# Performance work log

Measured on AMD Instinct MI355X. Metric: run time of the kernel, lower is better.

Reference implementation:

```python
import jax, jax.numpy as jnp
import numpy as np

B, NELEC, D, NION = 2048, 32, 512, 8
NSPIN = 2
N = NELEC // NSPIN  # electrons per spin = orbital-matrix size = 16


def setup_inputs() -> dict:
    key = jax.random.key(0)
    ks = jax.random.split(key, 6)
    eq_inputs = jax.random.normal(ks[0], (B, NELEC, D), jnp.float32)
    r_ei = jax.random.normal(ks[1], (B, NELEC, NION, 3), jnp.float32)
    # learned params (stacked over the 2 spins; equal split so shapes match)
    W_lin = jax.random.normal(ks[2], (NSPIN, 2 * D, N), jnp.float32) * (0.5 / np.sqrt(D))
    b_lin = jax.random.normal(ks[3], (NSPIN, N), jnp.float32) * 0.1
    A_env = jax.random.normal(ks[4], (NSPIN, 3, 3, NION, N), jnp.float32) * 0.3
    w_ion = jax.random.normal(ks[5], (NSPIN, NION, N), jnp.float32)
    return dict(eq_inputs=eq_inputs, r_ei=r_ei, W_lin=W_lin, b_lin=b_lin,
                A_env=A_env, w_ion=w_ion)


def reference(eq_inputs, r_ei, W_lin, b_lin, A_env, w_ion):
    """Per-particle determinant antiequivariance layer.

    For each spin s and particle p, a doubly-equivariant orbital matrix
    M_p[j, k] = (y_p . W1[:,k] + y_j . W2[:,k] + b[k]) * env[j, k]
    is built (pair-concat dense split into two einsums to avoid the (B,n,n,2d)
    intermediate), with anisotropic exponential envelopes
    env[j, k] = sum_I w_ion[I,k] * exp(-||A[:,:,I,k] @ r_ei[j,I,:]||).
    Output per spin: y_p * det(M_p), stacked over spins -> (B, 2, n, d).
    """
    b, nelec, d = eq_inputs.shape
    n = nelec // NSPIN
    x = eq_inputs.reshape(b, NSPIN, n, d)            # spin_split=2 equal split
    r = r_ei.reshape(b, NSPIN, n, r_ei.shape[-2], 3)
    W1, W2 = W_lin[:, :d], W_lin[:, d:]
    # linear (doubly equivariant) part: (B, S, n_p, n_j, n_k)
    lin_p = jnp.einsum('bspf,sfk->bspk', x, W1)
    lin_j = jnp.einsum('bsjf,sfk->bsjk', x, W2) + b_lin[None, :, None, :]
    lin = lin_p[:, :, :, None, :] + lin_j[:, :, None, :, :]
    # anisotropic exponential envelopes: exp(-||A (r - R)||), combined over ions
    ar = jnp.einsum('bsjip,spqik->bsjiqk', r, A_env)        # (B,S,n,I,3,k)
    env = jnp.exp(-jnp.sqrt(jnp.sum(ar * ar, axis=-2)))     # (B,S,n,I,k)
    env = jnp.einsum('bsjik,sik->bsjk', env, w_ion)         # (B,S,n_j,n_k)
    M = lin * env[:, :, None, :, :]                         # (B,S,n_p,n_j,n_k)
    dets = jnp.linalg.det(M)                                # (B,S,n_p)
    # y_p * det(M_p), per spin (stacked over the spin axis)
    return x * dets[..., None]                              # (B,S,n,d)
```

## Files before the change

### kernel.cpp

```cpp
#include <hip/hip_runtime.h>
#include <cstdint>
#include <cstddef>

#define NSPIN 2
#define NPART 16
#define DDIM  512
#define NION  8

#define RS_OFF    8192
#define LINP_OFF  (RS_OFF + 1536)
#define LINJ_OFF  (LINP_OFF + 1024)
#define ENV_OFF   (LINJ_OFF + 1280)
#define DETS_OFF  (ENV_OFF + 1280)
#define LDS_FLOATS (DETS_OFF + 64)
#define LDS_BYTES  (LDS_FLOATS * 4)

typedef short bf16x8 __attribute__((ext_vector_type(8)));
typedef float f32x4  __attribute__((ext_vector_type(4)));

__device__ __forceinline__ short bfc(float x) {
    unsigned u = __float_as_uint(x);
    u += 0x7FFFu + ((u >> 16) & 1u);
    return (short)(u >> 16);
}

#define DPPMAXU(k, ctrl) { unsigned o_ = (unsigned)__builtin_amdgcn_update_dpp(0, (int)(k), (ctrl), 0xF, 0xF, true); (k) = (k) > o_ ? (k) : o_; }

__global__ void __launch_bounds__(256, 3)
ppdet_kernel(const float* __restrict__ EQ, const float* __restrict__ RE,
             const float* __restrict__ WL, const float* __restrict__ BL,
             const float* __restrict__ AE, const float* __restrict__ WI,
             float* __restrict__ OUT)
{
    extern __shared__ float ls[];
    const int t  = threadIdx.x;
    const int s  = blockIdx.x >> 9;
    const int b0 = (blockIdx.x & 511) * 4;

    const int l  = t & 63;
    const int w  = t >> 6;
    const int c  = l & 15;
    const int h4 = l >> 4;
    const int jr = t & 15;
    const int ke = t >> 4;

    {
        const float* Wg = WL + (size_t)s * (2 * DDIM * NPART);
        ushort* wb = (ushort*)ls;
        #pragma unroll
        for (int it = 0; it < 8; ++it) {
            int slot = it * 256 + t;
            int half = slot >> 10;
            int ks   = (slot >> 6) & 15;
            int lane = slot & 63;
            int cc2  = lane & 15, hh = lane >> 4;
            const float* src = Wg + ((size_t)(half * 512 + ks * 32 + hh * 8)) * NPART + cc2;
            ushort u[8];
            #pragma unroll
            for (int e = 0; e < 8; ++e) u[e] = (ushort)bfc(src[e * NPART]);
            uint4 pk;
            pk.x = (unsigned)u[0] | ((unsigned)u[1] << 16);
            pk.y = (unsigned)u[2] | ((unsigned)u[3] << 16);
            pk.z = (unsigned)u[4] | ((unsigned)u[5] << 16);
            pk.w = (unsigned)u[6] | ((unsigned)u[7] << 16);
            *(uint4*)&wb[slot * 8] = pk;
        }
    }
    #pragma unroll
    for (int it = 0; it < 6; ++it) {
        int idx = it * 256 + t;
        int bi = idx / 384, rem = idx % 384;
        int e = rem >> 4, j = rem & 15;
        ls[RS_OFF + idx] = RE[((size_t)(b0 + bi) * 32 + s * 16 + j) * 24 + e];
    }
    __syncthreads();

    {
        const float* xg = EQ + ((size_t)(b0 + w) * 32 + s * 16 + c) * DDIM + h4 * 8;
        const ushort* wb = (const ushort*)ls;
        f32x4 accp = {0.f, 0.f, 0.f, 0.f}, accj = {0.f, 0.f, 0.f, 0.f};
        #pragma unroll
        for (int ks = 0; ks < 16; ++ks) {
            float4 a0 = *(const float4*)(xg + ks * 32);
            float4 a1 = *(const float4*)(xg + ks * 32 + 4);
            bf16x8 af;
            af[0] = bfc(a0.x); af[1] = bfc(a0.y); af[2] = bfc(a0.z); af[3] = bfc(a0.w);
            af[4] = bfc(a1.x); af[5] = bfc(a1.y); af[6] = bfc(a1.z); af[7] = bfc(a1.w);
            bf16x8 bf1 = *(const bf16x8*)(wb + (size_t)(ks * 64 + l) * 8);
            bf16x8 bf2 = *(const bf16x8*)(wb + (size_t)((16 + ks) * 64 + l) * 8);
            accp = __builtin_amdgcn_mfma_f32_16x16x32_bf16(af, bf1, accp, 0, 0, 0);
            accj = __builtin_amdgcn_mfma_f32_16x16x32_bf16(af, bf2, accj, 0, 0, 0);
        }
        const float blv = BL[s * NPART + c];
        #pragma unroll
        for (int q = 0; q < 4; ++q) {
            ls[LINP_OFF + (w * 16 + h4 * 4 + q) * 16 + c] = accp[q];
            ls[LINJ_OFF + (w * 16 + h4 * 4 + q) * 20 + c] = accj[q] + blv;
        }
    }

    {
        float G0[8], G1[8], G2[8], G3[8], G4[8], G5[8], wir[8];
        const float* Ag = AE + (size_t)s * (9 * NION * NPART);
        #pragma unroll
        for (int i = 0; i < 8; ++i) {
            float a00 = Ag[((0 * 3 + 0) * NION + i) * NPART + ke];
            float a01 = Ag[((0 * 3 + 1) * NION + i) * NPART + ke];
            float a02 = Ag[((0 * 3 + 2) * NION + i) * NPART + ke];
            float a10 = Ag[((1 * 3 + 0) * NION + i) * NPART + ke];
            float a11 = Ag[((1 * 3 + 1) * NION + i) * NPART + ke];
            float a12 = Ag[((1 * 3 + 2) * NION + i) * NPART + ke];
            float a20 = Ag[((2 * 3 + 0) * NION + i) * NPART + ke];
            float a21 = Ag[((2 * 3 + 1) * NION + i) * NPART + ke];
            float a22 = Ag[((2 * 3 + 2) * NION + i) * NPART + ke];
            G0[i] = a00 * a00 + a01 * a01 + a02 * a02;
            G1[i] = a10 * a10 + a11 * a11 + a12 * a12;
            G2[i] = a20 * a20 + a21 * a21 + a22 * a22;
            G3[i] = a00 * a10 + a01 * a11 + a02 * a12;
            G4[i] = a00 * a20 + a01 * a21 + a02 * a22;
            G5[i] = a10 * a20 + a11 * a21 + a12 * a22;
            wir[i] = WI[(size_t)s * (NION * NPART) + i * NPART + ke];
        }
        #pragma unroll
        for (int ib = 0; ib < 4; ++ib) {
            const float* rs = ls + RS_OFF + ib * 384;
            float ev = 0.f;
            #pragma unroll
            for (int i = 0; i < 8; ++i) {
                float r0 = rs[(i * 3 + 0) * 16 + jr];
                float r1 = rs[(i * 3 + 1) * 16 + jr];
                float r2 = rs[(i * 3 + 2) * 16 + jr];
                float ss = r0 * r0 * G0[i];
                ss = fmaf(r1 * r1, G1[i], ss);
                ss = fmaf(r2 * r2, G2[i], ss);
                float tcr = r0 * r1 * G3[i];
                tcr = fmaf(r0 * r2, G4[i], tcr);
                tcr = fmaf(r1 * r2, G5[i], tcr);
                ss = fmaf(2.f, tcr, ss);
                ss = fmaxf(ss, 0.f);
                ev = fmaf(wir[i], __expf(-__builtin_amdgcn_sqrtf(ss)), ev);
            }
            ls[ENV_OFF + (ib * 16 + jr) * 20 + ke] = ev;
        }
    }
    __syncthreads();

    const int lanebase4 = (t & 48) << 2;
    for (int ib = 0; ib < 4; ++ib) {
        float Mr[16];
        const float* lp = ls + LINP_OFF + (ib * 16 + ke) * 16;
        const float* lj = ls + LINJ_OFF + (ib * 16 + jr) * 20;
        const float* ev = ls + ENV_OFF  + (ib * 16 + jr) * 20;
        #pragma unroll
        for (int cq = 0; cq < 4; ++cq) {
            float4 a  = *(const float4*)(lp + cq * 4);
            float4 bb = *(const float4*)(lj + cq * 4);
            float4 e  = *(const float4*)(ev + cq * 4);
            Mr[cq * 4 + 0] = (a.x + bb.x) * e.x;
            Mr[cq * 4 + 1] = (a.y + bb.y) * e.y;
            Mr[cq * 4 + 2] = (a.z + bb.z) * e.z;
            Mr[cq * 4 + 3] = (a.w + bb.w) * e.w;
        }
        float detv = 1.f;
        unsigned sel = 0u;
        int inv = 0;
        bool msel = false;
        #pragma unroll
        for (int cc = 0; cc < 16; ++cc) {
            unsigned key = msel ? 0u
                : ((__float_as_uint(fabsf(Mr[cc])) & 0xFFFFFFF0u) | (unsigned)jr);
            DPPMAXU(key, 0x121); DPPMAXU(key, 0x122); DPPMAXU(key, 0x124); DPPMAXU(key, 0x128);
            const int idx = (int)(key & 15u);
            const bool ispiv = (jr == idx) && !msel;
            const int srcaddr = lanebase4 | (idx << 2);
            float Pr[16];
            #pragma unroll
            for (int k2 = cc; k2 < 16; ++k2)
                Pr[k2] = __int_as_float(__builtin_amdgcn_ds_bpermute(
                             srcaddr, __float_as_int(Mr[k2])));
            const float pv = Pr[cc];
            const float f = (msel || ispiv || pv == 0.f) ? 0.f
                          : Mr[cc] * __builtin_amdgcn_rcpf(pv);
            inv += __popc(sel >> (idx + 1));
            sel |= (1u << idx);
            msel = msel || ispiv;
            detv *= pv;
            #pragma unroll
            for (int k2 = cc + 1; k2 < 16; ++k2)
                Mr[k2] = fmaf(-f, Pr[k2], Mr[k2]);
        }
        if (inv & 1) detv = -detv;
        if (jr == 0) ls[DETS_OFF + ib * 16 + ke] = detv;
    }
    __syncthreads();

    #pragma unroll
    for (int ib = 0; ib < 4; ++ib) {
        const size_t base = ((size_t)(b0 + ib) * 32 + s * 16) * DDIM;
        #pragma unroll
        for (int i2 = 0; i2 < 8; ++i2) {
            int f4i = i2 * 256 + t;
            float dt = ls[DETS_OFF + ib * 16 + (f4i >> 7)];
            float4 xv = ((const float4*)(EQ + base))[f4i];
            float4 o = make_float4(xv.x * dt, xv.y * dt, xv.z * dt, xv.w * dt);
            ((float4*)(OUT + base))[f4i] = o;
        }
    }
}

extern "C" void kernel_launch(void* const* d_in, const int* in_sizes, int n_in,
                              void* d_out, int out_size, void* d_ws, size_t ws_size,
                              hipStream_t stream) {
    const float* EQ = (const float*)d_in[0];
    const float* RE = (const float*)d_in[1];
    const float* WL = (const float*)d_in[2];
    const float* BL = (const float*)d_in[3];
    const float* AE = (const float*)d_in[4];
    const float* WI = (const float*)d_in[5];
    float* OUT = (float*)d_out;
    (void)in_sizes; (void)n_in; (void)out_size; (void)d_ws; (void)ws_size;

    hipFuncSetAttribute((const void*)ppdet_kernel,
                        hipFuncAttributeMaxDynamicSharedMemorySize, LDS_BYTES);
    ppdet_kernel<<<dim3(1024), dim3(256), LDS_BYTES, stream>>>(EQ, RE, WL, BL, AE, WI, OUT);
}
```

Before: 86.39 us.

## Pre-pack bf16 weights in a separate prep kernel and read them from global memory

Moves the per-block fp32-to-bf16 conversion and MFMA-layout packing of W_lin into a small prep kernel that writes to the workspace once per call. The main kernel now loads the packed B-operands straight from global (L2-resident) memory instead of staging them in LDS. This removes 32 KB of LDS per block, allowing occupancy hints of 5 instead of 3. The GEMM loop is also restructured to batch loads four k-steps ahead of the MFMAs. In exchange it adds a second kernel launch and global-memory operand loads in the inner loop.

After: 76.33 us. -11.6%, faster.

```diff
diff --git a/kernel.cpp b/kernel.cpp
--- a/kernel.cpp
+++ b/kernel.cpp
@@ -7,8 +7,8 @@
 #define DDIM  512
 #define NION  8
 
-#define RS_OFF    8192
-#define LINP_OFF  (RS_OFF + 1536)
+#define RS_OFF    0
+#define LINP_OFF  1536
 #define LINJ_OFF  (LINP_OFF + 1024)
 #define ENV_OFF   (LINJ_OFF + 1280)
 #define DETS_OFF  (ENV_OFF + 1280)
@@ -26,9 +26,32 @@
 
 #define DPPMAXU(k, ctrl) { unsigned o_ = (unsigned)__builtin_amdgcn_update_dpp(0, (int)(k), (ctrl), 0xF, 0xF, true); (k) = (k) > o_ ? (k) : o_; }
 
-__global__ void __launch_bounds__(256, 3)
+__global__ void __launch_bounds__(256)
+prep_kernel(const float* __restrict__ WL, uint4* __restrict__ WS)
+{
+    int slot = blockIdx.x * 256 + threadIdx.x;
+    int spin = slot >> 11;
+    int rem  = slot & 2047;
+    int half = rem >> 10;
+    int ks   = (rem >> 6) & 15;
+    int lane = rem & 63;
+    int cc2  = lane & 15, hh = lane >> 4;
+    const float* src = WL + (size_t)spin * (2 * DDIM * NPART)
+                     + ((size_t)(half * 512 + ks * 32 + hh * 8)) * NPART + cc2;
+    ushort u[8];
+    #pragma unroll
+    for (int e = 0; e < 8; ++e) u[e] = (ushort)bfc(src[e * NPART]);
+    uint4 pk;
+    pk.x = (unsigned)u[0] | ((unsigned)u[1] << 16);
+    pk.y = (unsigned)u[2] | ((unsigned)u[3] << 16);
+    pk.z = (unsigned)u[4] | ((unsigned)u[5] << 16);
+    pk.w = (unsigned)u[6] | ((unsigned)u[7] << 16);
+    WS[slot] = pk;
+}
+
+__global__ void __launch_bounds__(256, 5)
 ppdet_kernel(const float* __restrict__ EQ, const float* __restrict__ RE,
-             const float* __restrict__ WL, const float* __restrict__ BL,
+             const uint4* __restrict__ WS, const float* __restrict__ BL,
              const float* __restrict__ AE, const float* __restrict__ WI,
              float* __restrict__ OUT)
 {
@@ -44,28 +67,6 @@
     const int jr = t & 15;
     const int ke = t >> 4;
 
-    {
-        const float* Wg = WL + (size_t)s * (2 * DDIM * NPART);
-        ushort* wb = (ushort*)ls;
-        #pragma unroll
-        for (int it = 0; it < 8; ++it) {
-            int slot = it * 256 + t;
-            int half = slot >> 10;
-            int ks   = (slot >> 6) & 15;
-            int lane = slot & 63;
-            int cc2  = lane & 15, hh = lane >> 4;
-            const float* src = Wg + ((size_t)(half * 512 + ks * 32 + hh * 8)) * NPART + cc2;
-            ushort u[8];
-            #pragma unroll
-            for (int e = 0; e < 8; ++e) u[e] = (ushort)bfc(src[e * NPART]);
-            uint4 pk;
-            pk.x = (unsigned)u[0] | ((unsigned)u[1] << 16);
-            pk.y = (unsigned)u[2] | ((unsigned)u[3] << 16);
-            pk.z = (unsigned)u[4] | ((unsigned)u[5] << 16);
-            pk.w = (unsigned)u[6] | ((unsigned)u[7] << 16);
-            *(uint4*)&wb[slot * 8] = pk;
-        }
-    }
     #pragma unroll
     for (int it = 0; it < 6; ++it) {
         int idx = it * 256 + t;
@@ -77,19 +78,29 @@
 
     {
         const float* xg = EQ + ((size_t)(b0 + w) * 32 + s * 16 + c) * DDIM + h4 * 8;
-        const ushort* wb = (const ushort*)ls;
+        const uint4* wb = WS + (size_t)s * 2048;
         f32x4 accp = {0.f, 0.f, 0.f, 0.f}, accj = {0.f, 0.f, 0.f, 0.f};
         #pragma unroll
-        for (int ks = 0; ks < 16; ++ks) {
-            float4 a0 = *(const float4*)(xg + ks * 32);
-            float4 a1 = *(const float4*)(xg + ks * 32 + 4);
-            bf16x8 af;
-            af[0] = bfc(a0.x); af[1] = bfc(a0.y); af[2] = bfc(a0.z); af[3] = bfc(a0.w);
-            af[4] = bfc(a1.x); af[5] = bfc(a1.y); af[6] = bfc(a1.z); af[7] = bfc(a1.w);
-            bf16x8 bf1 = *(const bf16x8*)(wb + (size_t)(ks * 64 + l) * 8);
-            bf16x8 bf2 = *(const bf16x8*)(wb + (size_t)((16 + ks) * 64 + l) * 8);
-            accp = __builtin_amdgcn_mfma_f32_16x16x32_bf16(af, bf1, accp, 0, 0, 0);
-            accj = __builtin_amdgcn_mfma_f32_16x16x32_bf16(af, bf2, accj, 0, 0, 0);
+        for (int kb = 0; kb < 4; ++kb) {
+            float4 xa[8];
+            uint4 w1v[4], w2v[4];
+            #pragma unroll
+            for (int u = 0; u < 4; ++u) {
+                xa[2 * u]     = *(const float4*)(xg + (kb * 4 + u) * 32);
+                xa[2 * u + 1] = *(const float4*)(xg + (kb * 4 + u) * 32 + 4);
+                w1v[u] = wb[(kb * 4 + u) * 64 + l];
+                w2v[u] = wb[(16 + kb * 4 + u) * 64 + l];
+            }
+            #pragma unroll
+            for (int u = 0; u < 4; ++u) {
+                bf16x8 af;
+                af[0] = bfc(xa[2 * u].x);     af[1] = bfc(xa[2 * u].y);
+                af[2] = bfc(xa[2 * u].z);     af[3] = bfc(xa[2 * u].w);
+                af[4] = bfc(xa[2 * u + 1].x); af[5] = bfc(xa[2 * u + 1].y);
+                af[6] = bfc(xa[2 * u + 1].z); af[7] = bfc(xa[2 * u + 1].w);
+                accp = __builtin_amdgcn_mfma_f32_16x16x32_bf16(af, *(bf16x8*)&w1v[u], accp, 0, 0, 0);
+                accj = __builtin_amdgcn_mfma_f32_16x16x32_bf16(af, *(bf16x8*)&w2v[u], accj, 0, 0, 0);
+            }
         }
         const float blv = BL[s * NPART + c];
         #pragma unroll
@@ -218,9 +229,9 @@
     const float* AE = (const float*)d_in[4];
     const float* WI = (const float*)d_in[5];
     float* OUT = (float*)d_out;
-    (void)in_sizes; (void)n_in; (void)out_size; (void)d_ws; (void)ws_size;
-
-    hipFuncSetAttribute((const void*)ppdet_kernel,
-                        hipFuncAttributeMaxDynamicSharedMemorySize, LDS_BYTES);
-    ppdet_kernel<<<dim3(1024), dim3(256), LDS_BYTES, stream>>>(EQ, RE, WL, BL, AE, WI, OUT);
-}
+    uint4* WS = (uint4*)d_ws;
+    (void)in_sizes; (void)n_in; (void)out_size; (void)ws_size;
+
+    prep_kernel<<<dim3(16), dim3(256), 0, stream>>>(WL, WS);
+    ppdet_kernel<<<dim3(1024), dim3(256), LDS_BYTES, stream>>>(EQ, RE, WS, BL, AE, WI, OUT);
+}
```
